# Kernel tuning notes

Measured on AMD Instinct MI355X. Metric: run time of the kernel, lower is better.

The kernel has to match this reference:

```python
import jax, jax.numpy as jnp
import numpy as np

# Geometry constants (match module defaults)
PCR = (0.0, -40.0, -3.0, 70.4, 40.0, 1.0)
VX, VY, VZ = 0.2, 0.2, 4.0
GX, GY, GZ = 352, 400, 1  # canvas_x/y/z per module's round() formulas
B = 2
N = 400000
C0, C1 = 64, 128
IN_CH = 10  # 4 raw + 3 cluster + 3 voxel-center
CANVAS = B * GZ * GY * GX
X_OFF = VX / 2 + PCR[0]
Y_OFF = VY / 2 + PCR[1]
Z_OFF = VZ / 2 + PCR[2]
BN_EPS = 1e-3


def setup_inputs() -> dict:
    key = jax.random.key(0)
    ks = jax.random.split(key, 8)
    x = jax.random.uniform(ks[0], (N,), minval=PCR[0], maxval=PCR[3] - 1e-3)
    y = jax.random.uniform(ks[1], (N,), minval=PCR[1], maxval=PCR[4] - 1e-3)
    z = jax.random.uniform(ks[2], (N,), minval=PCR[2], maxval=PCR[5] - 1e-3)
    inten = jax.random.uniform(ks[3], (N,))
    bidx = (jnp.arange(N) * B // N).astype(jnp.float32)  # sorted batch column
    points = jnp.stack([bidx, x, y, z, inten], axis=1).astype(jnp.float32)
    W0 = jax.random.normal(ks[4], (IN_CH, C0), dtype=jnp.float32) / np.sqrt(IN_CH)
    W1 = jax.random.normal(ks[5], (2 * C0, C1), dtype=jnp.float32) / np.sqrt(2 * C0)
    return {
        "points": points,
        "W0": W0, "g0": jnp.ones((C0,), jnp.float32), "b0": jnp.zeros((C0,), jnp.float32),
        "W1": W1, "g1": jnp.ones((C1,), jnp.float32), "b1": jnp.zeros((C1,), jnp.float32),
    }


def _vfe_layer(x, W, gamma, beta):
    # Linear(bias=False) -> BatchNorm1d(train-mode, eps=1e-3) -> ReLU
    h = x @ W
    mu = jnp.mean(h, axis=0)
    var = jnp.var(h, axis=0)
    h = (h - mu) * jax.lax.rsqrt(var + BN_EPS) * gamma + beta
    return jax.nn.relu(h)


def _forward(points, W0, g0, b0, W1, g1, b1):
    b = points[:, 0].astype(jnp.int32)
    xyz = points[:, 1:4]
    feats4 = points[:, 1:5]
    # dynamic voxelization: per-point voxel coordinates
    cx = jnp.clip(jnp.floor((points[:, 1] - PCR[0]) / VX), 0, GX - 1).astype(jnp.int32)
    cy = jnp.clip(jnp.floor((points[:, 2] - PCR[1]) / VY), 0, GY - 1).astype(jnp.int32)
    cz = jnp.clip(jnp.floor((points[:, 3] - PCR[2]) / VZ), 0, GZ - 1).astype(jnp.int32)
    vidx = ((b * GZ + cz) * GY + cy) * GX + cx  # flat canvas index per point

    count = jax.ops.segment_sum(jnp.ones((points.shape[0],), points.dtype), vidx,
                                num_segments=CANVAS)
    occupied = count > 0

    # cluster_scatter: mean of xyz per voxel, gathered back to points
    vox_mean = jax.ops.segment_sum(xyz, vidx, num_segments=CANVAS)
    vox_mean = vox_mean / jnp.maximum(count, 1.0)[:, None]
    f_cluster = xyz - vox_mean[vidx]

    # offset to voxel center
    vcen = jnp.stack([
        cx.astype(points.dtype) * VX + X_OFF,
        cy.astype(points.dtype) * VY + Y_OFF,
        cz.astype(points.dtype) * VZ + Z_OFF,
    ], axis=1)
    f_center = xyz - vcen

    feats = jnp.concatenate([feats4, f_cluster, f_center], axis=1)  # [N, 10]

    # VFE layer 0 -> scatter-max -> gather-back -> concat
    pf0 = _vfe_layer(feats, W0, g0, b0)  # [N, 64]
    vmax0 = jax.ops.segment_max(pf0, vidx, num_segments=CANVAS)
    vmax0 = jnp.where(occupied[:, None], vmax0, 0.0)
    feats1 = jnp.concatenate([pf0, vmax0[vidx]], axis=1)  # [N, 128]

    # VFE layer 1 -> final scatter-max over voxels
    pf1 = _vfe_layer(feats1, W1, g1, b1)  # [N, 128]
    vmax1 = jax.ops.segment_max(pf1, vidx, num_segments=CANVAS)
    voxel_feats = jnp.where(occupied[:, None], vmax1, 0.0)  # [CANVAS, 128] dense canvas
    return voxel_feats


def reference(points, W0, g0, b0, W1, g1, b1):
    return _forward(points, W0, g0, b0, W1, g1, b1)
```

## Files before the change

### kernel.cpp

```cpp
#include <hip/hip_runtime.h>
#include <hip/hip_fp16.h>
#include <stdint.h>

#define NPTS 400000
#define NVOX 281600
#define TPB  256
#define NBLK ((NPTS + TPB - 1) / TPB)
#define SCANB (NVOX / 256)
#define STRETCH 64
#define FBLK (NPTS / STRETCH)
#define SBLK2 1024

typedef _Float16 h8  __attribute__((ext_vector_type(8)));
typedef _Float16 h4v __attribute__((ext_vector_type(4)));
typedef float    f4  __attribute__((ext_vector_type(4)));

__device__ __forceinline__ int bin3(const float* __restrict__ pt,
                                    int& bx, int& by, int& bz) {
  float x = pt[1], y = pt[2], z = pt[3];
  bx = (int)fminf(fmaxf(floorf(x * 5.0f), 0.f), 351.f);
  by = (int)fminf(fmaxf(floorf((y + 40.f) * 5.0f), 0.f), 399.f);
  bz = (int)fminf(fmaxf(floorf((z + 3.f) * 0.25f), 0.f), 0.f);
  return (((int)pt[0] + bz) * 400 + by) * 352 + bx;
}

__device__ __forceinline__ int mkfeat(const float* __restrict__ pt,
    const float* __restrict__ vcnt, const float* __restrict__ vsx,
    const float* __restrict__ vsy, const float* __restrict__ vsz,
    float* f) {
  int bx, by, bz;
  int v = bin3(pt, bx, by, bz);
  float x = pt[1], y = pt[2], z = pt[3];
  float n = fmaxf(vcnt[v], 1.f);
  f[0] = x;  f[1] = y;  f[2] = z;  f[3] = pt[4];
  f[4] = x - vsx[v] / n;
  f[5] = y - vsy[v] / n;
  f[6] = z - vsz[v] / n;
  f[7] = x - (0.2f * (float)bx + 0.1f);
  f[8] = y - (0.2f * (float)by - 39.9f);
  f[9] = z - (4.0f * (float)bz - 1.0f);
  return v;
}

__global__ __launch_bounds__(256) void voxsum(const float* __restrict__ pts,
    float* __restrict__ vcnt, float* __restrict__ vsx,
    float* __restrict__ vsy, float* __restrict__ vsz) {
  int p = blockIdx.x * TPB + threadIdx.x;
  if (p >= NPTS) return;
  const float* pt = pts + (size_t)p * 5;
  int bx, by, bz;
  int v = bin3(pt, bx, by, bz);
  atomicAdd(&vcnt[v], 1.f);
  atomicAdd(&vsx[v], pt[1]);
  atomicAdd(&vsy[v], pt[2]);
  atomicAdd(&vsz[v], pt[3]);
}

__global__ __launch_bounds__(256) void bn0stats(const float* __restrict__ pts,
    const float* __restrict__ vcnt, const float* __restrict__ vsx,
    const float* __restrict__ vsy, const float* __restrict__ vsz,
    const float* __restrict__ W0,
    double* __restrict__ gs, double* __restrict__ gq) {
  __shared__ float bs[4][64], bq[4][64];
  int t = threadIdx.x, wv = t >> 6, ln = t & 63;
  int p = blockIdx.x * TPB + t;
  bool ok = p < NPTS;
  const float* pt = pts + (size_t)(ok ? p : 0) * 5;
  float f[10];
  mkfeat(pt, vcnt, vsx, vsy, vsz, f);
  for (int c = 0; c < 64; ++c) {
    float h = f[0] * W0[c];
    #pragma unroll
    for (int i = 1; i < 10; ++i) h = fmaf(f[i], W0[i * 64 + c], h);
    h = ok ? h : 0.f;
    float q = h * h;
    #pragma unroll
    for (int m = 1; m < 64; m <<= 1) {
      h += __shfl_xor(h, m, 64);
      q += __shfl_xor(q, m, 64);
    }
    if (ln == 0) { bs[wv][c] = h; bq[wv][c] = q; }
  }
  __syncthreads();
  if (t < 64) {
    atomicAdd(&gs[t], (double)bs[0][t] + bs[1][t] + bs[2][t] + bs[3][t]);
    atomicAdd(&gq[t], (double)bq[0][t] + bq[1][t] + bq[2][t] + bq[3][t]);
  }
}

__global__ void bnfold(const double* __restrict__ gs, const double* __restrict__ gq,
                       const float* __restrict__ gam, const float* __restrict__ bet,
                       float* __restrict__ sc, float* __restrict__ sh, int C) {
  int c = threadIdx.x;
  if (c >= C) return;
  double mu  = gs[c] / (double)NPTS;
  double var = gq[c] / (double)NPTS - mu * mu;
  double s = (double)gam[c] / sqrt(var + 1e-3);
  sc[c] = (float)s;
  sh[c] = (float)((double)bet[c] - mu * s);
}

__global__ __launch_bounds__(256) void scan1(const float* __restrict__ vcnt,
    unsigned int* __restrict__ voxloc, unsigned int* __restrict__ bsum) {
  __shared__ unsigned int s[256];
  int t = threadIdx.x;
  int i = blockIdx.x * 256 + t;
  unsigned int val = (unsigned int)vcnt[i];
  s[t] = val;
  __syncthreads();
  for (int off = 1; off < 256; off <<= 1) {
    unsigned int add = (t >= off) ? s[t - off] : 0u;
    __syncthreads();
    s[t] += add;
    __syncthreads();
  }
  voxloc[i] = s[t] - val;
  if (t == 255) bsum[blockIdx.x] = s[t];
}

__global__ void scan2(const unsigned int* __restrict__ bsum,
                      unsigned int* __restrict__ bexc) {
  if (threadIdx.x != 0) return;
  unsigned int run = 0;
  for (int b = 0; b < SCANB; ++b) { bexc[b] = run; run += bsum[b]; }
}

__global__ __launch_bounds__(256) void scatter(const float* __restrict__ pts,
    const unsigned int* __restrict__ voxloc, const unsigned int* __restrict__ bexc,
    unsigned int* __restrict__ cursor, unsigned int* __restrict__ plist,
    unsigned int* __restrict__ vsort) {
  int p = blockIdx.x * TPB + threadIdx.x;
  if (p >= NPTS) return;
  int bx, by, bz;
  int v = bin3(pts + (size_t)p * 5, bx, by, bz);
  unsigned int pos = voxloc[v] + bexc[v >> 8] + atomicAdd(&cursor[v], 1u);
  plist[pos] = (unsigned int)p;
  vsort[pos] = (unsigned int)v;
}

__global__ __launch_bounds__(256) void vmax0_stretch(const float* __restrict__ pts,
    const float* __restrict__ vcnt, const float* __restrict__ vsx,
    const float* __restrict__ vsy, const float* __restrict__ vsz,
    const unsigned int* __restrict__ voxloc, const unsigned int* __restrict__ bexc,
    const unsigned int* __restrict__ plist,
    const float* __restrict__ W0, const float* __restrict__ sc0,
    const float* __restrict__ sh0, float* __restrict__ vmax) {
  __shared__ float sf[STRETCH][12];
  __shared__ int   svid[STRETCH];
  __shared__ float pf[STRETCH][64];
  int t = threadIdx.x;
  unsigned int sbeg = blockIdx.x * STRETCH;

  if (t < STRETCH) {
    unsigned int pidx = plist[sbeg + t];
    svid[t] = mkfeat(pts + (size_t)pidx * 5, vcnt, vsx, vsy, vsz, &sf[t][0]);
  }
  __syncthreads();
  for (int idx = t; idx < STRETCH * 64; idx += TPB) {
    int pt_ = idx >> 6, k = idx & 63;
    float h = sf[pt_][0] * W0[k];
    #pragma unroll
    for (int i = 1; i < 10; ++i) h = fmaf(sf[pt_][i], W0[i * 64 + k], h);
    pf[pt_][k] = fmaxf(fmaf(h, sc0[k], sh0[k]), 0.f);
  }
  __syncthreads();

  if (t < 64) {
    int curv = -1; float curm = 0.f;
    for (int i = 0; i < STRETCH; ++i) {
      int v = svid[i];
      if (v != curv) {
        if (curv >= 0) {
          unsigned int vstart = voxloc[curv] + bexc[curv >> 8];
          unsigned int n = (unsigned int)vcnt[curv];
          if (vstart >= sbeg && vstart + n <= sbeg + STRETCH)
            vmax[(size_t)curv * 64 + t] = curm;
          else
            atomicMax((unsigned int*)&vmax[(size_t)curv * 64 + t],
                      __float_as_uint(curm));
        }
        curv = v;
        curm = pf[i][t];
      } else {
        curm = fmaxf(curm, pf[i][t]);
      }
    }
    if (curv >= 0) {
      unsigned int vstart = voxloc[curv] + bexc[curv >> 8];
      unsigned int n = (unsigned int)vcnt[curv];
      if (vstart >= sbeg && vstart + n <= sbeg + STRETCH)
        vmax[(size_t)curv * 64 + t] = curm;
      else
        atomicMax((unsigned int*)&vmax[(size_t)curv * 64 + t],
                  __float_as_uint(curm));
    }
  }
}

__global__ __launch_bounds__(256) void wconv(const float* __restrict__ W1,
                                             _Float16* __restrict__ Wf) {
  int idx = blockIdx.x * 256 + threadIdx.x;
  if (idx >= 32 * 64 * 8) return;
  int j = idx & 7, l = (idx >> 3) & 63, f = idx >> 9;
  int ks = f & 3, ntile = f >> 2;
  int k = ks * 32 + ((j >> 2) * 16) + 4 * (l >> 4) + (j & 3);
  int n = ntile * 16 + (l & 15);
  Wf[idx] = (_Float16)W1[k * 128 + n];
}

__device__ __forceinline__ h8 lda(const _Float16* __restrict__ r, int k0) {
  h4v lo = *(const h4v*)(r + k0);
  h4v hi = *(const h4v*)(r + k0 + 16);
  h8 a;
  a[0] = lo[0]; a[1] = lo[1]; a[2] = lo[2]; a[3] = lo[3];
  a[4] = hi[0]; a[5] = hi[1]; a[6] = hi[2]; a[7] = hi[3];
  return a;
}

__device__ __forceinline__ void emit_tile(f4 C, int ptb, int ch,
    _Float16* __restrict__ h1o, float& sf_, float& qf_) {
  float v0 = C[0], v1 = C[1], v2 = C[2], v3 = C[3];
  h1o[(size_t)(ptb + 0) * 128 + ch] = (_Float16)v0;
  h1o[(size_t)(ptb + 1) * 128 + ch] = (_Float16)v1;
  h1o[(size_t)(ptb + 2) * 128 + ch] = (_Float16)v2;
  h1o[(size_t)(ptb + 3) * 128 + ch] = (_Float16)v3;
  sf_ += (v0 + v1) + (v2 + v3);
  qf_ = fmaf(v0, v0, fmaf(v1, v1, fmaf(v2, v2, fmaf(v3, v3, qf_))));
}

__global__ __launch_bounds__(256) void gemm1m(const float* __restrict__ pts,
    const float* __restrict__ vcnt, const float* __restrict__ vsx,
    const float* __restrict__ vsy, const float* __restrict__ vsz,
    const unsigned int* __restrict__ plist,
    const float* __restrict__ W0, const float* __restrict__ sc0,
    const float* __restrict__ sh0, const float* __restrict__ vmax,
    const _Float16* __restrict__ Wf,
    double* __restrict__ gs, double* __restrict__ gq,
    _Float16* __restrict__ h1out) {
  __shared__ float sf[STRETCH][12];
  __shared__ int   svid[STRETCH];
  __shared__ __align__(16) _Float16 fh[64][140];

  int t = threadIdx.x;
  int w = t >> 6, l = t & 63;
  int lm = l & 15, lg = l >> 4;

  const h8* wfv = (const h8*)Wf;
  h8 B00 = wfv[((w * 2 + 0) * 4 + 0) * 64 + l];
  h8 B01 = wfv[((w * 2 + 0) * 4 + 1) * 64 + l];
  h8 B02 = wfv[((w * 2 + 0) * 4 + 2) * 64 + l];
  h8 B03 = wfv[((w * 2 + 0) * 4 + 3) * 64 + l];
  h8 B10 = wfv[((w * 2 + 1) * 4 + 0) * 64 + l];
  h8 B11 = wfv[((w * 2 + 1) * 4 + 1) * 64 + l];
  h8 B12 = wfv[((w * 2 + 1) * 4 + 2) * 64 + l];
  h8 B13 = wfv[((w * 2 + 1) * 4 + 3) * 64 + l];

  double sd0 = 0, sd1 = 0, qd0 = 0, qd1 = 0;

  for (int tile = blockIdx.x; tile < FBLK; tile += gridDim.x) {
    unsigned int sbeg = tile * STRETCH;
    if (t < STRETCH) {
      unsigned int pidx = plist[sbeg + t];
      svid[t] = mkfeat(pts + (size_t)pidx * 5, vcnt, vsx, vsy, vsz, &sf[t][0]);
    }
    __syncthreads();
    for (int idx = t; idx < STRETCH * 64; idx += TPB) {
      int p_ = idx >> 6, k = idx & 63;
      float h = sf[p_][0] * W0[k];
      #pragma unroll
      for (int i = 1; i < 10; ++i) h = fmaf(sf[p_][i], W0[i * 64 + k], h);
      fh[p_][k] = (_Float16)fmaxf(fmaf(h, sc0[k], sh0[k]), 0.f);
    }
    for (int idx = t; idx < STRETCH * 64; idx += TPB) {
      int p_ = idx >> 6, k = idx & 63;
      fh[p_][64 + k] = (_Float16)vmax[(size_t)svid[p_] * 64 + k];
    }
    __syncthreads();

    f4 C00 = {0,0,0,0}, C01 = {0,0,0,0}, C10 = {0,0,0,0}, C11 = {0,0,0,0};
    f4 C20 = {0,0,0,0}, C21 = {0,0,0,0}, C30 = {0,0,0,0}, C31 = {0,0,0,0};

    #define DO_MT(mt, CA, CB) {                                              \
      const _Float16* r = &fh[(mt) * 16 + lm][0];                            \
      h8 A0 = lda(r, 0 * 32 + 4 * lg);                                       \
      h8 A1 = lda(r, 1 * 32 + 4 * lg);                                       \
      h8 A2 = lda(r, 2 * 32 + 4 * lg);                                       \
      h8 A3 = lda(r, 3 * 32 + 4 * lg);                                       \
      CA = __builtin_amdgcn_mfma_f32_16x16x32_f16(A0, B00, CA, 0, 0, 0);     \
      CA = __builtin_amdgcn_mfma_f32_16x16x32_f16(A1, B01, CA, 0, 0, 0);     \
      CA = __builtin_amdgcn_mfma_f32_16x16x32_f16(A2, B02, CA, 0, 0, 0);     \
      CA = __builtin_amdgcn_mfma_f32_16x16x32_f16(A3, B03, CA, 0, 0, 0);     \
      CB = __builtin_amdgcn_mfma_f32_16x16x32_f16(A0, B10, CB, 0, 0, 0);     \
      CB = __builtin_amdgcn_mfma_f32_16x16x32_f16(A1, B11, CB, 0, 0, 0);     \
      CB = __builtin_amdgcn_mfma_f32_16x16x32_f16(A2, B12, CB, 0, 0, 0);     \
      CB = __builtin_amdgcn_mfma_f32_16x16x32_f16(A3, B13, CB, 0, 0, 0); }
    DO_MT(0, C00, C01)
    DO_MT(1, C10, C11)
    DO_MT(2, C20, C21)
    DO_MT(3, C30, C31)
    #undef DO_MT

    float s0f = 0, q0f = 0, s1f = 0, q1f = 0;
    int ch0 = w * 32 + lm, ch1 = w * 32 + 16 + lm;
    emit_tile(C00, sbeg + 0 * 16 + lg * 4, ch0, h1out, s0f, q0f);
    emit_tile(C01, sbeg + 0 * 16 + lg * 4, ch1, h1out, s1f, q1f);
    emit_tile(C10, sbeg + 1 * 16 + lg * 4, ch0, h1out, s0f, q0f);
    emit_tile(C11, sbeg + 1 * 16 + lg * 4, ch1, h1out, s1f, q1f);
    emit_tile(C20, sbeg + 2 * 16 + lg * 4, ch0, h1out, s0f, q0f);
    emit_tile(C21, sbeg + 2 * 16 + lg * 4, ch1, h1out, s1f, q1f);
    emit_tile(C30, sbeg + 3 * 16 + lg * 4, ch0, h1out, s0f, q0f);
    emit_tile(C31, sbeg + 3 * 16 + lg * 4, ch1, h1out, s1f, q1f);
    sd0 += (double)s0f; qd0 += (double)q0f;
    sd1 += (double)s1f; qd1 += (double)q1f;
    __syncthreads();
  }

  sd0 += __shfl_xor(sd0, 16, 64); sd0 += __shfl_xor(sd0, 32, 64);
  qd0 += __shfl_xor(qd0, 16, 64); qd0 += __shfl_xor(qd0, 32, 64);
  sd1 += __shfl_xor(sd1, 16, 64); sd1 += __shfl_xor(sd1, 32, 64);
  qd1 += __shfl_xor(qd1, 16, 64); qd1 += __shfl_xor(qd1, 32, 64);
  if (lg == 0) {
    atomicAdd(&gs[w * 32 + lm], sd0);
    atomicAdd(&gq[w * 32 + lm], qd0);
    atomicAdd(&gs[w * 32 + 16 + lm], sd1);
    atomicAdd(&gq[w * 32 + 16 + lm], qd1);
  }
}

__global__ __launch_bounds__(128) void final_cheap(
    const unsigned int* __restrict__ vsort,
    const unsigned int* __restrict__ voxloc, const unsigned int* __restrict__ bexc,
    const float* __restrict__ vcnt, const __half* __restrict__ h1,
    const float* __restrict__ sc1, const float* __restrict__ sh1,
    float* __restrict__ outp) {
  int t = threadIdx.x;
  unsigned int sbeg = blockIdx.x * STRETCH;
  float s = sc1[t], b = sh1[t];
  int curv = -1; float curm = 0.f;
  for (int i = 0; i < STRETCH; ++i) {
    int v = (int)vsort[sbeg + i];
    float h = __half2float(h1[(size_t)(sbeg + i) * 128 + t]);
    float val = fmaxf(fmaf(h, s, b), 0.f);
    if (v != curv) {
      if (curv >= 0) {
        unsigned int vstart = voxloc[curv] + bexc[curv >> 8];
        unsigned int n = (unsigned int)vcnt[curv];
        if (vstart >= sbeg && vstart + n <= sbeg + STRETCH)
          outp[(size_t)curv * 128 + t] = curm;
        else
          atomicMax((unsigned int*)&outp[(size_t)curv * 128 + t],
                    __float_as_uint(curm));
      }
      curv = v;
      curm = val;
    } else {
      curm = fmaxf(curm, val);
    }
  }
  if (curv >= 0) {
    unsigned int vstart = voxloc[curv] + bexc[curv >> 8];
    unsigned int n = (unsigned int)vcnt[curv];
    if (vstart >= sbeg && vstart + n <= sbeg + STRETCH)
      outp[(size_t)curv * 128 + t] = curm;
    else
      atomicMax((unsigned int*)&outp[(size_t)curv * 128 + t],
                __float_as_uint(curm));
  }
}

#define TILE_STAGE(sbeg_)                                                    \
  if (t < STRETCH) {                                                         \
    unsigned int pidx = plist[(sbeg_) + t];                                  \
    svid[t] = mkfeat(pts + (size_t)pidx * 5, vcnt, vsx, vsy, vsz, &sf[t][0]);\
  }                                                                          \
  __syncthreads();                                                           \
  for (int idx = t; idx < STRETCH * 64; idx += TPB) {                        \
    int pt_ = idx >> 6, k = idx & 63;                                        \
    float h = sf[pt_][0] * W0[k];                                            \
    _Pragma("unroll")                                                        \
    for (int i = 1; i < 10; ++i) h = fmaf(sf[pt_][i], W0[i * 64 + k], h);    \
    sfeat[pt_][k] = fmaxf(fmaf(h, sc0[k], sh0[k]), 0.f);                     \
  }                                                                          \
  for (int idx = t; idx < STRETCH * 64; idx += TPB) {                        \
    int pt_ = idx >> 6, k = idx & 63;                                        \
    sfeat[pt_][64 + k] = vmax[(size_t)svid[pt_] * 64 + k];                   \
  }                                                                          \
  __syncthreads();

#define TILE_GEMM()                                                          \
  const float* r0 = sfeat[pg * 8 + 0];                                       \
  const float* r1 = sfeat[pg * 8 + 1];                                       \
  const float* r2 = sfeat[pg * 8 + 2];                                       \
  const float* r3 = sfeat[pg * 8 + 3];                                       \
  const float* r4 = sfeat[pg * 8 + 4];                                       \
  const float* r5 = sfeat[pg * 8 + 5];                                       \
  const float* r6 = sfeat[pg * 8 + 6];                                       \
  const float* r7 = sfeat[pg * 8 + 7];                                       \
  float4 A0 = {0,0,0,0}, A1 = {0,0,0,0}, A2 = {0,0,0,0}, A3 = {0,0,0,0};     \
  float4 A4 = {0,0,0,0}, A5 = {0,0,0,0}, A6 = {0,0,0,0}, A7 = {0,0,0,0};     \
  _Pragma("unroll 8")                                                        \
  for (int k = 0; k < 128; ++k) {                                            \
    float4 w = *reinterpret_cast<const float4*>(W1 + (size_t)k * 128 + cb*4);\
    float p0 = r0[k], p1_ = r1[k], p2 = r2[k], p3 = r3[k];                   \
    float p4 = r4[k], p5 = r5[k], p6 = r6[k], p7 = r7[k];                    \
    A0.x = fmaf(p0, w.x, A0.x); A0.y = fmaf(p0, w.y, A0.y);                  \
    A0.z = fmaf(p0, w.z, A0.z); A0.w = fmaf(p0, w.w, A0.w);                  \
    A1.x = fmaf(p1_, w.x, A1.x); A1.y = fmaf(p1_, w.y, A1.y);                \
    A1.z = fmaf(p1_, w.z, A1.z); A1.w = fmaf(p1_, w.w, A1.w);                \
    A2.x = fmaf(p2, w.x, A2.x); A2.y = fmaf(p2, w.y, A2.y);                  \
    A2.z = fmaf(p2, w.z, A2.z); A2.w = fmaf(p2, w.w, A2.w);                  \
    A3.x = fmaf(p3, w.x, A3.x); A3.y = fmaf(p3, w.y, A3.y);                  \
    A3.z = fmaf(p3, w.z, A3.z); A3.w = fmaf(p3, w.w, A3.w);                  \
    A4.x = fmaf(p4, w.x, A4.x); A4.y = fmaf(p4, w.y, A4.y);                  \
    A4.z = fmaf(p4, w.z, A4.z); A4.w = fmaf(p4, w.w, A4.w);                  \
    A5.x = fmaf(p5, w.x, A5.x); A5.y = fmaf(p5, w.y, A5.y);                  \
    A5.z = fmaf(p5, w.z, A5.z); A5.w = fmaf(p5, w.w, A5.w);                  \
    A6.x = fmaf(p6, w.x, A6.x); A6.y = fmaf(p6, w.y, A6.y);                  \
    A6.z = fmaf(p6, w.z, A6.z); A6.w = fmaf(p6, w.w, A6.w);                  \
    A7.x = fmaf(p7, w.x, A7.x); A7.y = fmaf(p7, w.y, A7.y);                  \
    A7.z = fmaf(p7, w.z, A7.z); A7.w = fmaf(p7, w.w, A7.w);                  \
  }

__global__ __launch_bounds__(256) void gemm1s_f32(const float* __restrict__ pts,
    const float* __restrict__ vcnt, const float* __restrict__ vsx,
    const float* __restrict__ vsy, const float* __restrict__ vsz,
    const unsigned int* __restrict__ plist,
    const float* __restrict__ W0, const float* __restrict__ sc0,
    const float* __restrict__ sh0, const float* __restrict__ vmax,
    const float* __restrict__ W1,
    double* __restrict__ gs, double* __restrict__ gq) {
  union SM {
    struct { float sf[STRETCH][12]; int svid[STRETCH]; float sfeat[STRETCH][128]; } a;
    struct { double lsum[8 * 128]; double lsq[8 * 128]; } b;
  };
  __shared__ SM sm;
  auto& sf = sm.a.sf;
  auto& svid = sm.a.svid;
  auto& sfeat = sm.a.sfeat;

  int t = threadIdx.x;
  int pg = t >> 5, cb = t & 31;
  double sd0 = 0, sd1 = 0, sd2 = 0, sd3 = 0;
  double qd0 = 0, qd1 = 0, qd2 = 0, qd3 = 0;

  for (int tile = blockIdx.x; tile < FBLK; tile += gridDim.x) {
    unsigned int sbeg = tile * STRETCH;
    TILE_STAGE(sbeg)
    TILE_GEMM()
    sd0 += (double)A0.x + (double)A1.x + (double)A2.x + (double)A3.x
         + (double)A4.x + (double)A5.x + (double)A6.x + (double)A7.x;
    sd1 += (double)A0.y + (double)A1.y + (double)A2.y + (double)A3.y
         + (double)A4.y + (double)A5.y + (double)A6.y + (double)A7.y;
    sd2 += (double)A0.z + (double)A1.z + (double)A2.z + (double)A3.z
         + (double)A4.z + (double)A5.z + (double)A6.z + (double)A7.z;
    sd3 += (double)A0.w + (double)A1.w + (double)A2.w + (double)A3.w
         + (double)A4.w + (double)A5.w + (double)A6.w + (double)A7.w;
    qd0 += (double)A0.x*A0.x + (double)A1.x*A1.x + (double)A2.x*A2.x + (double)A3.x*A3.x
         + (double)A4.x*A4.x + (double)A5.x*A5.x + (double)A6.x*A6.x + (double)A7.x*A7.x;
    qd1 += (double)A0.y*A0.y + (double)A1.y*A1.y + (double)A2.y*A2.y + (double)A3.y*A3.y
         + (double)A4.y*A4.y + (double)A5.y*A5.y + (double)A6.y*A6.y + (double)A7.y*A7.y;
    qd2 += (double)A0.z*A0.z + (double)A1.z*A1.z + (double)A2.z*A2.z + (double)A3.z*A3.z
         + (double)A4.z*A4.z + (double)A5.z*A5.z + (double)A6.z*A6.z + (double)A7.z*A7.z;
    qd3 += (double)A0.w*A0.w + (double)A1.w*A1.w + (double)A2.w*A2.w + (double)A3.w*A3.w
         + (double)A4.w*A4.w + (double)A5.w*A5.w + (double)A6.w*A6.w + (double)A7.w*A7.w;
    __syncthreads();
  }

  int c = cb * 4;
  sm.b.lsum[pg * 128 + c + 0] = sd0;  sm.b.lsq[pg * 128 + c + 0] = qd0;
  sm.b.lsum[pg * 128 + c + 1] = sd1;  sm.b.lsq[pg * 128 + c + 1] = qd1;
  sm.b.lsum[pg * 128 + c + 2] = sd2;  sm.b.lsq[pg * 128 + c + 2] = qd2;
  sm.b.lsum[pg * 128 + c + 3] = sd3;  sm.b.lsq[pg * 128 + c + 3] = qd3;
  __syncthreads();
  if (t < 128) {
    double S = 0, Q = 0;
    #pragma unroll
    for (int j = 0; j < 8; ++j) { S += sm.b.lsum[j * 128 + t]; Q += sm.b.lsq[j * 128 + t]; }
    atomicAdd(&gs[t], S);
    atomicAdd(&gq[t], Q);
  }
}

__global__ __launch_bounds__(256) void final2(const float* __restrict__ pts,
    const float* __restrict__ vcnt, const float* __restrict__ vsx,
    const float* __restrict__ vsy, const float* __restrict__ vsz,
    const unsigned int* __restrict__ voxloc, const unsigned int* __restrict__ bexc,
    const unsigned int* __restrict__ plist,
    const float* __restrict__ W0, const float* __restrict__ sc0,
    const float* __restrict__ sh0, const float* __restrict__ vmax,
    const float* __restrict__ W1, const float* __restrict__ sc1,
    const float* __restrict__ sh1, float* __restrict__ outp) {
  __shared__ float sf[STRETCH][12];
  __shared__ int   svid[STRETCH];
  __shared__ float sfeat[STRETCH][128];

  int t = threadIdx.x;
  int pg = t >> 5, cb = t & 31;
  unsigned int sbeg = blockIdx.x * STRETCH;

  TILE_STAGE(sbeg)
  TILE_GEMM()
  __syncthreads();

  int c = cb * 4;
  float4 s1v = *reinterpret_cast<const float4*>(sc1 + c);
  float4 h1v = *reinterpret_cast<const float4*>(sh1 + c);
  #define BNST(Aj, j)                                                        \
    { float4 P;                                                              \
      P.x = fmaxf(fmaf(Aj.x, s1v.x, h1v.x), 0.f);                            \
      P.y = fmaxf(fmaf(Aj.y, s1v.y, h1v.y), 0.f);                            \
      P.z = fmaxf(fmaf(Aj.z, s1v.z, h1v.z), 0.f);                            \
      P.w = fmaxf(fmaf(Aj.w, s1v.w, h1v.w), 0.f);                            \
      *reinterpret_cast<float4*>(&sfeat[pg * 8 + j][c]) = P; }
  BNST(A0, 0) BNST(A1, 1) BNST(A2, 2) BNST(A3, 3)
  BNST(A4, 4) BNST(A5, 5) BNST(A6, 6) BNST(A7, 7)
  #undef BNST
  __syncthreads();

  if (t < 128) {
    int curv = -1; float curm = 0.f;
    for (int i = 0; i < STRETCH; ++i) {
      int v = svid[i];
      if (v != curv) {
        if (curv >= 0) {
          unsigned int vstart = voxloc[curv] + bexc[curv >> 8];
          unsigned int n = (unsigned int)vcnt[curv];
          if (vstart >= sbeg && vstart + n <= sbeg + STRETCH)
            outp[(size_t)curv * 128 + t] = curm;
          else
            atomicMax((unsigned int*)&outp[(size_t)curv * 128 + t],
                      __float_as_uint(curm));
        }
        curv = v;
        curm = sfeat[i][t];
      } else {
        curm = fmaxf(curm, sfeat[i][t]);
      }
    }
    if (curv >= 0) {
      unsigned int vstart = voxloc[curv] + bexc[curv >> 8];
      unsigned int n = (unsigned int)vcnt[curv];
      if (vstart >= sbeg && vstart + n <= sbeg + STRETCH)
        outp[(size_t)curv * 128 + t] = curm;
      else
        atomicMax((unsigned int*)&outp[(size_t)curv * 128 + t],
                  __float_as_uint(curm));
    }
  }
}

extern "C" void kernel_launch(void* const* d_in, const int* in_sizes, int n_in,
                              void* d_out, int out_size, void* d_ws, size_t ws_size,
                              hipStream_t stream) {
  const float* pts = (const float*)d_in[0];
  const float* W0  = (const float*)d_in[1];
  const float* g0  = (const float*)d_in[2];
  const float* b0  = (const float*)d_in[3];
  const float* W1  = (const float*)d_in[4];
  const float* g1  = (const float*)d_in[5];
  const float* b1  = (const float*)d_in[6];

  char* base = (char*)d_ws;
  double* stats = (double*)base;
  float*  fold  = (float*)(base + 3072);
  float*  vcnt  = (float*)(base + 4608);
  float*  vsx   = vcnt + NVOX;
  float*  vsy   = vsx + NVOX;
  float*  vsz   = vsy + NVOX;
  float*  vmax  = vsz + NVOX;
  unsigned int* voxloc = (unsigned int*)(vmax + (size_t)NVOX * 64);
  unsigned int* cursor = voxloc + NVOX;
  unsigned int* plist  = cursor + NVOX;
  unsigned int* vsort  = plist + NPTS;
  unsigned int* bsum   = vsort + NPTS;
  unsigned int* bexc   = bsum + SCANB;
  _Float16* Wf = (_Float16*)(bexc + SCANB);
  _Float16* h1 = Wf + 32 * 64 * 8;
  size_t need_fast = (size_t)((char*)h1 - base) + (size_t)NPTS * 128 * sizeof(_Float16);
  bool fast = ws_size >= need_fast;

  double* s0 = stats,       *q0 = stats + 64;
  double* s1 = stats + 128, *q1 = stats + 256;
  float* sc0 = fold,       *sh0 = fold + 64;
  float* sc1 = fold + 128, *sh1 = fold + 256;

  hipMemsetAsync(stats, 0, 3072, stream);
  hipMemsetAsync(vcnt, 0, (size_t)4 * NVOX * sizeof(float), stream);
  hipMemsetAsync(vmax, 0, (size_t)NVOX * 64 * sizeof(float), stream);
  hipMemsetAsync(cursor, 0, (size_t)NVOX * sizeof(unsigned int), stream);
  hipMemsetAsync(d_out, 0, (size_t)out_size * sizeof(float), stream);

  voxsum<<<NBLK, TPB, 0, stream>>>(pts, vcnt, vsx, vsy, vsz);
  scan1<<<SCANB, 256, 0, stream>>>(vcnt, voxloc, bsum);
  scan2<<<1, 64, 0, stream>>>(bsum, bexc);
  scatter<<<NBLK, TPB, 0, stream>>>(pts, voxloc, bexc, cursor, plist, vsort);
  bn0stats<<<NBLK, TPB, 0, stream>>>(pts, vcnt, vsx, vsy, vsz, W0, s0, q0);
  bnfold<<<1, 64, 0, stream>>>(s0, q0, g0, b0, sc0, sh0, 64);
  vmax0_stretch<<<FBLK, TPB, 0, stream>>>(pts, vcnt, vsx, vsy, vsz, voxloc, bexc,
                                          plist, W0, sc0, sh0, vmax);
  if (fast) {
    wconv<<<64, 256, 0, stream>>>(W1, Wf);
    gemm1m<<<SBLK2, TPB, 0, stream>>>(pts, vcnt, vsx, vsy, vsz, plist,
                                      W0, sc0, sh0, vmax, Wf, s1, q1, h1);
    bnfold<<<1, 128, 0, stream>>>(s1, q1, g1, b1, sc1, sh1, 128);
    final_cheap<<<FBLK, 128, 0, stream>>>(vsort, voxloc, bexc, vcnt,
                                          (const __half*)h1, sc1, sh1,
                                          (float*)d_out);
  } else {
    gemm1s_f32<<<SBLK2, TPB, 0, stream>>>(pts, vcnt, vsx, vsy, vsz, plist,
                                          W0, sc0, sh0, vmax, W1, s1, q1);
    bnfold<<<1, 128, 0, stream>>>(s1, q1, g1, b1, sc1, sh1, 128);
    final2<<<FBLK, TPB, 0, stream>>>(pts, vcnt, vsx, vsy, vsz, voxloc, bexc,
                                     plist, W0, sc0, sh0, vmax, W1, sc1, sh1,
                                     (float*)d_out);
  }
}
```

Measured before the change: 459.5 us.

## Replace full canvas memsets with selective zeroing kernel and vectorize final scatter-max

Drops the full-buffer memsets of the output canvas and the vmax buffer. A new prep kernel zeroes only the output rows of empty voxels, plus the output and vmax rows of voxels whose point run crosses a stretch boundary. Rows of interior voxels are left for later kernels, which overwrite them directly. The final scatter-max kernel now gives one 64-lane wave per stretch, packs four stretches per block, and has each lane handle two channels with half2/float2 loads and stores. This trades a large blind memory fill for a per-voxel pass with strided 512-byte writes, and relies on every interior voxel being fully written by downstream kernels.

```diff
diff --git a/kernel.cpp b/kernel.cpp
--- a/kernel.cpp
+++ b/kernel.cpp
@@ -125,6 +125,30 @@
   for (int b = 0; b < SCANB; ++b) { bexc[b] = run; run += bsum[b]; }
 }
 
+__global__ __launch_bounds__(256) void prep(const float* __restrict__ vcnt,
+    const unsigned int* __restrict__ voxloc, const unsigned int* __restrict__ bexc,
+    float* __restrict__ vmax, float* __restrict__ outp) {
+  int v = blockIdx.x * 256 + threadIdx.x;
+  int n = (int)vcnt[v];
+  f4 z = {0, 0, 0, 0};
+  if (n == 0) {
+    f4* o = (f4*)(outp + (size_t)v * 128);
+    #pragma unroll
+    for (int i = 0; i < 32; ++i) o[i] = z;
+    return;
+  }
+  unsigned int vstart = voxloc[v] + bexc[v >> 8];
+  bool interior = ((vstart & (STRETCH - 1)) + (unsigned)n) <= STRETCH;
+  if (!interior) {
+    f4* o = (f4*)(outp + (size_t)v * 128);
+    #pragma unroll
+    for (int i = 0; i < 32; ++i) o[i] = z;
+    f4* m = (f4*)(vmax + (size_t)v * 64);
+    #pragma unroll
+    for (int i = 0; i < 16; ++i) m[i] = z;
+  }
+}
+
 __global__ __launch_bounds__(256) void scatter(const float* __restrict__ pts,
     const unsigned int* __restrict__ voxloc, const unsigned int* __restrict__ bexc,
     unsigned int* __restrict__ cursor, unsigned int* __restrict__ plist,
@@ -327,45 +351,47 @@
   }
 }
 
-__global__ __launch_bounds__(128) void final_cheap(
+__global__ __launch_bounds__(256) void final_cheap(
     const unsigned int* __restrict__ vsort,
     const unsigned int* __restrict__ voxloc, const unsigned int* __restrict__ bexc,
-    const float* __restrict__ vcnt, const __half* __restrict__ h1,
+    const float* __restrict__ vcnt, const _Float16* __restrict__ h1,
     const float* __restrict__ sc1, const float* __restrict__ sh1,
     float* __restrict__ outp) {
-  int t = threadIdx.x;
-  unsigned int sbeg = blockIdx.x * STRETCH;
-  float s = sc1[t], b = sh1[t];
-  int curv = -1; float curm = 0.f;
+  int t = threadIdx.x, w = t >> 6, l = t & 63;
+  int s = blockIdx.x * 4 + w;
+  if (s >= FBLK) return;
+  unsigned int sbeg = (unsigned int)s * STRETCH;
+  float2 sv = *(const float2*)(sc1 + 2 * l);
+  float2 bv = *(const float2*)(sh1 + 2 * l);
+
+  int curv = -1; float m0 = 0.f, m1 = 0.f;
+  #define FLUSH()                                                            \
+    { unsigned int vstart = voxloc[curv] + bexc[curv >> 8];                  \
+      unsigned int n = (unsigned int)vcnt[curv];                             \
+      if (vstart >= sbeg && vstart + n <= sbeg + STRETCH) {                  \
+        *(float2*)(outp + (size_t)curv * 128 + 2 * l) = make_float2(m0, m1); \
+      } else {                                                               \
+        atomicMax((unsigned int*)&outp[(size_t)curv * 128 + 2 * l],          \
+                  __float_as_uint(m0));                                      \
+        atomicMax((unsigned int*)&outp[(size_t)curv * 128 + 2 * l + 1],      \
+                  __float_as_uint(m1));                                      \
+      } }
   for (int i = 0; i < STRETCH; ++i) {
     int v = (int)vsort[sbeg + i];
-    float h = __half2float(h1[(size_t)(sbeg + i) * 128 + t]);
-    float val = fmaxf(fmaf(h, s, b), 0.f);
+    __half2 hv = *(const __half2*)(h1 + (size_t)(sbeg + i) * 128 + 2 * l);
+    float2 hf = __half22float2(hv);
+    float v0 = fmaxf(fmaf(hf.x, sv.x, bv.x), 0.f);
+    float v1 = fmaxf(fmaf(hf.y, sv.y, bv.y), 0.f);
     if (v != curv) {
-      if (curv >= 0) {
-        unsigned int vstart = voxloc[curv] + bexc[curv >> 8];
-        unsigned int n = (unsigned int)vcnt[curv];
-        if (vstart >= sbeg && vstart + n <= sbeg + STRETCH)
-          outp[(size_t)curv * 128 + t] = curm;
-        else
-          atomicMax((unsigned int*)&outp[(size_t)curv * 128 + t],
-                    __float_as_uint(curm));
-      }
-      curv = v;
-      curm = val;
+      if (curv >= 0) FLUSH()
+      curv = v; m0 = v0; m1 = v1;
     } else {
-      curm = fmaxf(curm, val);
-    }
-  }
-  if (curv >= 0) {
-    unsigned int vstart = voxloc[curv] + bexc[curv >> 8];
-    unsigned int n = (unsigned int)vcnt[curv];
-    if (vstart >= sbeg && vstart + n <= sbeg + STRETCH)
-      outp[(size_t)curv * 128 + t] = curm;
-    else
-      atomicMax((unsigned int*)&outp[(size_t)curv * 128 + t],
-                __float_as_uint(curm));
-  }
+      m0 = fmaxf(m0, v0);
+      m1 = fmaxf(m1, v1);
+    }
+  }
+  if (curv >= 0) FLUSH()
+  #undef FLUSH
 }
 
 #define TILE_STAGE(sbeg_)                                                    \
@@ -586,13 +612,12 @@
 
   hipMemsetAsync(stats, 0, 3072, stream);
   hipMemsetAsync(vcnt, 0, (size_t)4 * NVOX * sizeof(float), stream);
-  hipMemsetAsync(vmax, 0, (size_t)NVOX * 64 * sizeof(float), stream);
   hipMemsetAsync(cursor, 0, (size_t)NVOX * sizeof(unsigned int), stream);
-  hipMemsetAsync(d_out, 0, (size_t)out_size * sizeof(float), stream);
 
   voxsum<<<NBLK, TPB, 0, stream>>>(pts, vcnt, vsx, vsy, vsz);
   scan1<<<SCANB, 256, 0, stream>>>(vcnt, voxloc, bsum);
   scan2<<<1, 64, 0, stream>>>(bsum, bexc);
+  prep<<<SCANB, 256, 0, stream>>>(vcnt, voxloc, bexc, vmax, (float*)d_out);
   scatter<<<NBLK, TPB, 0, stream>>>(pts, voxloc, bexc, cursor, plist, vsort);
   bn0stats<<<NBLK, TPB, 0, stream>>>(pts, vcnt, vsx, vsy, vsz, W0, s0, q0);
   bnfold<<<1, 64, 0, stream>>>(s0, q0, g0, b0, sc0, sh0, 64);
@@ -603,9 +628,8 @@
     gemm1m<<<SBLK2, TPB, 0, stream>>>(pts, vcnt, vsx, vsy, vsz, plist,
                                       W0, sc0, sh0, vmax, Wf, s1, q1, h1);
     bnfold<<<1, 128, 0, stream>>>(s1, q1, g1, b1, sc1, sh1, 128);
-    final_cheap<<<FBLK, 128, 0, stream>>>(vsort, voxloc, bexc, vcnt,
-                                          (const __half*)h1, sc1, sh1,
-                                          (float*)d_out);
+    final_cheap<<<(FBLK + 3) / 4, 256, 0, stream>>>(vsort, voxloc, bexc, vcnt,
+                                                    h1, sc1, sh1, (float*)d_out);
   } else {
     gemm1s_f32<<<SBLK2, TPB, 0, stream>>>(pts, vcnt, vsx, vsy, vsz, plist,
                                           W0, sc0, sh0, vmax, W1, s1, q1);
```

Result: faster. 420.1 us (-8.6%).
